# Optimization experiments

Hardware: AMD Instinct MI355X
Metric: run time of the kernel (lower is better)

Reference implementation:

```python
import jax, jax.numpy as jnp
import numpy as np

N = 8192      # num_nodes
B = 16        # batch
IN_DIM = 2    # input_dim
HID = 64      # hid_dim
K = 2         # diffusion_steps
DEG = 16
E = N * DEG
F = IN_DIM + HID            # concat(input, state) feature dim
NUM_MAT = 2 * K + 1         # dual random walk: 2 matrices * K steps + identity


def _spmm(vals, rows, cols, x):
    # sparse [N,N] @ dense [N,M]: y[rows[e]] += vals[e] * x[cols[e]]
    return jax.ops.segment_sum(vals[:, None] * x[cols], rows, num_segments=N)


def _diff_conv(x, W, b, edge_src, edge_dst, vals1, vals2):
    # x: [B, N, F] -> [B, N*out_dim]; Chebyshev-like diffusion recursion
    x0 = jnp.transpose(x, (1, 2, 0)).reshape(N, F * B)  # [N, F*B]
    xs = [x0]
    # matrix 1 = D_out^-1 A (edges src->dst), matrix 2 = D_in^-1 A^T (edges dst->src)
    for rows, cols, vals in ((edge_src, edge_dst, vals1), (edge_dst, edge_src, vals2)):
        x1 = _spmm(vals, rows, cols, x0)
        xs.append(x1)
        xp, xc = x0, x1
        for _ in range(2, K + 1):
            xn = 2.0 * _spmm(vals, rows, cols, xc) - xp
            xs.append(xn)
            xp, xc = xc, xn
    xstk = jnp.stack(xs, 0).reshape(NUM_MAT, N, F, B)
    xstk = jnp.transpose(xstk, (3, 1, 2, 0)).reshape(B * N, F * NUM_MAT)
    out = xstk @ W + b  # [B*N, out_dim]
    return out.reshape(B, -1)


def setup_inputs() -> dict:
    key = jax.random.key(0)
    k = jax.random.split(key, 8)
    inputs = jax.random.normal(k[0], (B, N * IN_DIM), jnp.float32)
    state = jax.random.normal(k[1], (B, N * HID), jnp.float32)
    edge_src = jax.random.randint(k[2], (E,), 0, N)
    edge_dst = jax.random.randint(k[3], (E,), 0, N)
    a = jax.random.uniform(k[4], (E,), jnp.float32) + 0.1  # positive edge weights
    dout = jax.ops.segment_sum(a, edge_src, num_segments=N)
    din = jax.ops.segment_sum(a, edge_dst, num_segments=N)
    vals1 = a / jnp.where(dout > 0, dout, 1.0)[edge_src]  # random-walk normalize A
    vals2 = a / jnp.where(din > 0, din, 1.0)[edge_dst]    # random-walk normalize A^T
    std_g = 1.414 * np.sqrt(2.0 / (F * NUM_MAT + 2 * HID)).astype(np.float32)
    std_c = 1.414 * np.sqrt(2.0 / (F * NUM_MAT + HID)).astype(np.float32)
    W_gate = jax.random.normal(k[5], (F * NUM_MAT, 2 * HID), jnp.float32) * std_g
    b_gate = jnp.zeros((2 * HID,), jnp.float32)
    W_cand = jax.random.normal(k[6], (F * NUM_MAT, HID), jnp.float32) * std_c
    b_cand = jnp.zeros((HID,), jnp.float32)
    return dict(inputs=inputs, state=state, edge_src=edge_src, edge_dst=edge_dst,
                vals1=vals1, vals2=vals2, W_gate=W_gate, b_gate=b_gate,
                W_cand=W_cand, b_cand=b_cand)


def reference(inputs, state, edge_src, edge_dst, vals1, vals2,
              W_gate, b_gate, W_cand, b_cand):
    i = inputs.reshape(B, N, IN_DIM)
    s = state.reshape(B, N, HID)
    x = jnp.concatenate([i, s], axis=2)  # [B, N, F]
    value = jax.nn.sigmoid(_diff_conv(x, W_gate, b_gate, edge_src, edge_dst, vals1, vals2))
    value = value.reshape(B, N, 2 * HID)
    r = value[..., :HID].reshape(B, N * HID)
    u = value[..., HID:].reshape(B, N * HID)
    rs = (r * state).reshape(B, N, HID)
    xc = jnp.concatenate([i, rs], axis=2)
    c = jnp.tanh(_diff_conv(xc, W_cand, b_cand, edge_src, edge_dst, vals1, vals2))
    new_state = u * state + (1.0 - u) * c
    return (new_state, new_state)
```

## Files before the change

kernel.cpp:

```cpp
#include <hip/hip_runtime.h>
#include <cstddef>
#include <cstdint>

#define NNODES 8192
#define BATCH  16
#define HID    64
#define NEDGE  131072
#define SN     524288
#define OUTHALF 8388608
#define FP2    72
#define SLABU  1152
#define NSTR   5760
#define NSTR4  720
#define XCS4   144
#define KP2    384
#define GN     8
#define CWB    288
#define BXB    18432

typedef __attribute__((ext_vector_type(8))) short bf16x8;
typedef __attribute__((ext_vector_type(4))) float f32x4;

static __device__ __forceinline__ float bf2f(ushort u) {
    union { uint32_t i; float f; } c; c.i = ((uint32_t)u) << 16; return c.f;
}
static __device__ __forceinline__ ushort f2bf(float f) {
    union { float f; uint32_t i; } c; c.f = f;
    uint32_t lsb = (c.i >> 16) & 1;
    return (ushort)((c.i + 0x7fffu + lsb) >> 16);
}


__global__ void hist_kernel(const int* __restrict__ src, const int* __restrict__ dst,
                            int* __restrict__ c1, int* __restrict__ c2) {
    int e = blockIdx.x * 256 + threadIdx.x;
    if (e < NEDGE) {
        atomicAdd(&c1[src[e]], 1);
        atomicAdd(&c2[dst[e]], 1);
    }
}

__global__ __launch_bounds__(1024) void scan_kernel(const int* __restrict__ counts1,
                                                    const int* __restrict__ counts2,
                                                    int* __restrict__ rowptr1,
                                                    int* __restrict__ rowptr2,
                                                    int* __restrict__ cursor1,
                                                    int* __restrict__ cursor2) {
    const int* counts = blockIdx.x ? counts2 : counts1;
    int* rowptr       = blockIdx.x ? rowptr2 : rowptr1;
    int* cursor       = blockIdx.x ? cursor2 : cursor1;
    __shared__ int sh[1024];
    int tid = threadIdx.x;
    int base = tid * 8;
    int local[8];
    int sum = 0;
#pragma unroll
    for (int j = 0; j < 8; ++j) { local[j] = counts[base + j]; sum += local[j]; }
    sh[tid] = sum;
    __syncthreads();
    for (int off = 1; off < 1024; off <<= 1) {
        int v = (tid >= off) ? sh[tid - off] : 0;
        __syncthreads();
        sh[tid] += v;
        __syncthreads();
    }
    int p = sh[tid] - sum;
#pragma unroll
    for (int j = 0; j < 8; ++j) {
        cursor[base + j] = p;
        p += local[j];
        rowptr[base + j + 1] = p;
    }
    if (tid == 0) rowptr[0] = 0;
}

__global__ void scatter_kernel(const int* __restrict__ src, const int* __restrict__ dst,
                               const float* __restrict__ v1, const float* __restrict__ v2,
                               int* __restrict__ cur1, int* __restrict__ cur2,
                               int* __restrict__ cols1, float* __restrict__ valsC1,
                               int* __restrict__ cols2, float* __restrict__ valsC2) {
    int e = blockIdx.x * 256 + threadIdx.x;
    if (e < NEDGE) {
        int r1 = src[e];
        int p1 = atomicAdd(&cur1[r1], 1);
        cols1[p1] = dst[e];
        valsC1[p1] = v1[e];
        int r2 = dst[e];
        int p2 = atomicAdd(&cur2[r2], 1);
        cols2[p2] = src[e];
        valsC2[p2] = v2[e];
    }
}


__global__ void prep_kernel(const float* __restrict__ Wg, const float* __restrict__ Wc,
                            ushort* __restrict__ WgT, ushort* __restrict__ WcT,
                            const float* __restrict__ inputs, const float* __restrict__ state,
                            uint* __restrict__ Xb_u, uint* __restrict__ Xc_u) {
    if (blockIdx.x < CWB) {
        int i = blockIdx.x * 256 + threadIdx.x;
        if (i >= 192 * KP2) return;
        int col = i / KP2, k2 = i - col * KP2;
        int m = k2 / FP2, f = k2 - m * FP2;
        bool valid = (m < 5) && (f < 66);
        int ko = f * 5 + m;
        if (col < 128) {
            WgT[col * KP2 + k2] = valid ? f2bf(Wg[ko * 128 + col]) : (ushort)0;
        } else {
            int c = col - 128;
            WcT[c * KP2 + k2] = valid ? f2bf(Wc[ko * 64 + c]) : (ushort)0;
        }
        return;
    }
    int t = (blockIdx.x - CWB) * 256 + threadIdx.x;
    if (t >= NNODES * BATCH * 36) return;
    int n = t / 576;
    int r = t - n * 576;
    int b = r / 36;
    int j = r - b * 36;
    int f0 = 2 * j;
    uint val = 0;
    if (f0 == 0) {
        float v0 = inputs[(size_t)b * (NNODES * 2) + n * 2 + 0];
        float v1 = inputs[(size_t)b * (NNODES * 2) + n * 2 + 1];
        val = (uint)f2bf(v0) | ((uint)f2bf(v1) << 16);
    } else if (f0 < 66) {
        float v0 = state[(size_t)b * SN + n * HID + (f0 - 2)];
        float v1 = state[(size_t)b * SN + n * HID + (f0 - 1)];
        val = (uint)f2bf(v0) | ((uint)f2bf(v1) << 16);
    }
    Xb_u[(size_t)n * 2880 + r] = val;
    if (f0 == 0 || f0 >= 66) Xc_u[t] = val;
}


static __device__ __forceinline__ void fma8(float* acc, uint4 d, float v) {
    acc[0] += v * bf2f((ushort)(d.x));  acc[1] += v * bf2f((ushort)(d.x >> 16));
    acc[2] += v * bf2f((ushort)(d.y));  acc[3] += v * bf2f((ushort)(d.y >> 16));
    acc[4] += v * bf2f((ushort)(d.z));  acc[5] += v * bf2f((ushort)(d.z >> 16));
    acc[6] += v * bf2f((ushort)(d.w));  acc[7] += v * bf2f((ushort)(d.w >> 16));
}

static __device__ __forceinline__ uint4 blend_pack8(const float* acc, uint4 p,
                                                    float alpha, float beta) {
    float o[8];
    o[0] = alpha * acc[0] + beta * bf2f((ushort)(p.x));
    o[1] = alpha * acc[1] + beta * bf2f((ushort)(p.x >> 16));
    o[2] = alpha * acc[2] + beta * bf2f((ushort)(p.y));
    o[3] = alpha * acc[3] + beta * bf2f((ushort)(p.y >> 16));
    o[4] = alpha * acc[4] + beta * bf2f((ushort)(p.z));
    o[5] = alpha * acc[5] + beta * bf2f((ushort)(p.z >> 16));
    o[6] = alpha * acc[6] + beta * bf2f((ushort)(p.w));
    o[7] = alpha * acc[7] + beta * bf2f((ushort)(p.w >> 16));
    uint4 r;
    r.x = (uint32_t)f2bf(o[0]) | ((uint32_t)f2bf(o[1]) << 16);
    r.y = (uint32_t)f2bf(o[2]) | ((uint32_t)f2bf(o[3]) << 16);
    r.z = (uint32_t)f2bf(o[4]) | ((uint32_t)f2bf(o[5]) << 16);
    r.w = (uint32_t)f2bf(o[6]) | ((uint32_t)f2bf(o[7]) << 16);
    return r;
}

__global__ __launch_bounds__(128) void spmm_dual(
        const int* __restrict__ rp1, const int* __restrict__ c1, const float* __restrict__ v1,
        const uint4* __restrict__ x1,
        const int* __restrict__ rp2, const int* __restrict__ c2, const float* __restrict__ v2,
        const uint4* __restrict__ x2,
        int xs,
        const uint4* __restrict__ xp, int ps,
        uint4* __restrict__ y1, uint4* __restrict__ y2, int ys,
        float alpha, float beta) {
    int bid = blockIdx.x;
    int half = bid >> 13;
    int n = bid & 8191;
    const int* rowptr = half ? rp2 : rp1;
    const int* cols   = half ? c2 : c1;
    const float* vals = half ? v2 : v1;
    const uint4* x    = half ? x2 : x1;
    uint4* y          = half ? y2 : y1;

    int t = threadIdx.x;
    int s = rowptr[n], e = rowptr[n + 1];
    float a0[8] = {0, 0, 0, 0, 0, 0, 0, 0};
    float a1[8] = {0, 0, 0, 0, 0, 0, 0, 0};
    bool tail = t < 16;
    int t2 = 128 + t;
    for (int i = s; i < e; i += 8) {
        int   c[8];
        float v[8];
#pragma unroll
        for (int k = 0; k < 8; ++k) {
            int ii = i + k;
            bool ok = ii < e;
            int idx = ok ? ii : s;
            c[k] = cols[idx];
            v[k] = ok ? vals[idx] : 0.f;
        }
        uint4 d[8];
#pragma unroll
        for (int k = 0; k < 8; ++k) d[k] = x[(size_t)c[k] * xs + t];
        uint4 d2[8];
        if (tail) {
#pragma unroll
            for (int k = 0; k < 8; ++k) d2[k] = x[(size_t)c[k] * xs + t2];
        }
#pragma unroll
        for (int k = 0; k < 8; ++k) fma8(a0, d[k], v[k]);
        if (tail) {
#pragma unroll
            for (int k = 0; k < 8; ++k) fma8(a1, d2[k], v[k]);
        }
    }
    uint4* yb = y + (size_t)n * ys;
    const uint4* xpb = xp + (size_t)n * ps;
    uint4 p0 = (beta != 0.f) ? xpb[t] : make_uint4(0, 0, 0, 0);
    yb[t] = blend_pack8(a0, p0, alpha, beta);
    if (tail) {
        uint4 p1 = (beta != 0.f) ? xpb[t2] : make_uint4(0, 0, 0, 0);
        yb[t2] = blend_pack8(a1, p1, alpha, beta);
    }
}


__global__ __launch_bounds__(256, 2) void gate_mfma(const ushort* __restrict__ Xb,
                                                    const ushort* __restrict__ WgT,
                                                    const float* __restrict__ bg,
                                                    float* __restrict__ U,
                                                    ushort* __restrict__ Xc) {
    int tid = threadIdx.x;
    int wave = tid >> 6, lane = tid & 63;
    int row = lane & 15, quad = lane >> 4;
    int c0 = wave * 32 + row;
    int c1 = c0 + 16;

    bf16x8 w0[12], w1[12];
#pragma unroll
    for (int kt = 0; kt < 12; ++kt) {
        w0[kt] = *(const bf16x8*)(WgT + (size_t)c0 * KP2 + kt * 32 + quad * 8);
        w1[kt] = *(const bf16x8*)(WgT + (size_t)c1 * KP2 + kt * 32 + quad * 8);
    }
    float bias0 = bg[c0], bias1 = bg[c1];

    int offA[11];
#pragma unroll
    for (int kt = 0; kt < 11; ++kt) {
        int j = 4 * kt + quad;
        int m = j / 9;
        int f0 = 8 * (j - 9 * m);
        offA[kt] = m * SLABU + row * FP2 + f0;
    }
    int off11 = 4 * SLABU + row * FP2 + 64;
    const bf16x8 zf = {0, 0, 0, 0, 0, 0, 0, 0};

    int nodeBase = blockIdx.x * GN;
    bf16x8 aC[12], aN[12];
    {
        const ushort* An = Xb + (size_t)nodeBase * NSTR;
#pragma unroll
        for (int kt = 0; kt < 11; ++kt) aC[kt] = *(const bf16x8*)(An + offA[kt]);
        aC[11] = (quad == 0) ? *(const bf16x8*)(An + off11) : zf;
    }
    for (int g = 0; g < GN; ++g) {
        int n = nodeBase + g;
        const ushort* An = Xb + (size_t)n * NSTR;
        if (g + 1 < GN) {
            const ushort* An2 = An + NSTR;
#pragma unroll
            for (int kt = 0; kt < 11; ++kt) aN[kt] = *(const bf16x8*)(An2 + offA[kt]);
            aN[11] = (quad == 0) ? *(const bf16x8*)(An2 + off11) : zf;
        }
        f32x4 acc0 = {0.f, 0.f, 0.f, 0.f};
        f32x4 acc1 = {0.f, 0.f, 0.f, 0.f};
#pragma unroll
        for (int kt = 0; kt < 12; ++kt) {
            acc0 = __builtin_amdgcn_mfma_f32_16x16x32_bf16(aC[kt], w0[kt], acc0, 0, 0, 0);
            acc1 = __builtin_amdgcn_mfma_f32_16x16x32_bf16(aC[kt], w1[kt], acc1, 0, 0, 0);
        }
#pragma unroll
        for (int r = 0; r < 4; ++r) {
            int b = quad * 4 + r;
            float v0 = 1.f / (1.f + __expf(-(acc0[r] + bias0)));
            float v1 = 1.f / (1.f + __expf(-(acc1[r] + bias1)));
            if (wave < 2) {
                float s0 = bf2f(An[b * FP2 + 2 + c0]);
                float s1 = bf2f(An[b * FP2 + 2 + c1]);
                Xc[(size_t)n * SLABU + b * FP2 + 2 + c0] = f2bf(v0 * s0);
                Xc[(size_t)n * SLABU + b * FP2 + 2 + c1] = f2bf(v1 * s1);
            } else {
                U[(size_t)b * SN + n * HID + (c0 - HID)] = v0;
                U[(size_t)b * SN + n * HID + (c1 - HID)] = v1;
            }
        }
        if (g + 1 < GN) {
#pragma unroll
            for (int kt = 0; kt < 12; ++kt) aC[kt] = aN[kt];
        }
    }
}


__global__ __launch_bounds__(256, 2) void cand_mfma(const ushort* __restrict__ Xb,
                                                    const ushort* __restrict__ Xc,
                                                    const ushort* __restrict__ WcT,
                                                    const float* __restrict__ bc,
                                                    const float* __restrict__ state,
                                                    const float* U,
                                                    float* out) {
    int tid = threadIdx.x;
    int wave = tid >> 6, lane = tid & 63;
    int row = lane & 15, quad = lane >> 4;
    int c = wave * 16 + row;

    bf16x8 w[12];
#pragma unroll
    for (int kt = 0; kt < 12; ++kt)
        w[kt] = *(const bf16x8*)(WcT + (size_t)c * KP2 + kt * 32 + quad * 8);
    float bias = bc[c];

    int offA[11];
#pragma unroll
    for (int kt = 0; kt < 11; ++kt) {
        int j = 4 * kt + quad;
        int m = j / 9;
        int f0 = 8 * (j - 9 * m);
        offA[kt] = m * SLABU + row * FP2 + f0;
    }
    int off11 = 4 * SLABU + row * FP2 + 64;
    const bf16x8 zf = {0, 0, 0, 0, 0, 0, 0, 0};

    int nodeBase = blockIdx.x * GN;
    bf16x8 aC[12], aN[12];
    auto loadA = [&](int n, bf16x8* a) {
        const ushort* AnB = Xb + (size_t)n * NSTR;
        const ushort* AnC = Xc + (size_t)n * SLABU;
#pragma unroll
        for (int kt = 0; kt < 11; ++kt) {
            const ushort* bp = (kt < 2) ? AnC
                             : (kt == 2 ? (quad == 0 ? AnC : AnB) : AnB);
            a[kt] = *(const bf16x8*)(bp + offA[kt]);
        }
        a[11] = (quad == 0) ? *(const bf16x8*)(AnB + off11) : zf;
    };
    loadA(nodeBase, aC);
    for (int g = 0; g < GN; ++g) {
        int n = nodeBase + g;
        if (g + 1 < GN) loadA(n + 1, aN);
        f32x4 acc = {0.f, 0.f, 0.f, 0.f};
#pragma unroll
        for (int kt = 0; kt < 12; ++kt)
            acc = __builtin_amdgcn_mfma_f32_16x16x32_bf16(aC[kt], w[kt], acc, 0, 0, 0);
#pragma unroll
        for (int r = 0; r < 4; ++r) {
            int b = quad * 4 + r;
            float pre = acc[r] + bias;
            float cv = 1.f - 2.f / (__expf(2.f * pre) + 1.f);
            size_t idx = (size_t)b * SN + n * HID + c;
            float uv = U[idx];
            float s = state[idx];
            float ns = uv * s + (1.f - uv) * cv;
            out[idx] = ns;
            out[OUTHALF + idx] = ns;
        }
        if (g + 1 < GN) {
#pragma unroll
            for (int kt = 0; kt < 12; ++kt) aC[kt] = aN[kt];
        }
    }
}


extern "C" void kernel_launch(void* const* d_in, const int* in_sizes, int n_in,
                              void* d_out, int out_size, void* d_ws, size_t ws_size,
                              hipStream_t stream) {
    const float* inputs = (const float*)d_in[0];
    const float* state  = (const float*)d_in[1];
    const int*   esrc   = (const int*)d_in[2];
    const int*   edst   = (const int*)d_in[3];
    const float* v1     = (const float*)d_in[4];
    const float* v2     = (const float*)d_in[5];
    const float* Wg     = (const float*)d_in[6];
    const float* bg     = (const float*)d_in[7];
    const float* Wc     = (const float*)d_in[8];
    const float* bc     = (const float*)d_in[9];
    float* out = (float*)d_out;

    char* ws = (char*)d_ws;
    size_t off = 0;
    auto alloc = [&](size_t bytes) -> void* {
        void* p = ws + off;
        off += (bytes + 255) & ~(size_t)255;
        return p;
    };
    ushort* Xb     = (ushort*)alloc((size_t)NNODES * NSTR * 2);
    ushort* Xc     = (ushort*)alloc((size_t)NNODES * SLABU * 2);
    ushort* WgT    = (ushort*)alloc((size_t)128 * KP2 * 2);
    ushort* WcT    = (ushort*)alloc((size_t)64 * KP2 * 2);
    int*   counts1 = (int*)alloc(NNODES * 4);
    int*   counts2 = (int*)alloc(NNODES * 4);
    int*   rowptr1 = (int*)alloc((NNODES + 1) * 4);
    int*   rowptr2 = (int*)alloc((NNODES + 1) * 4);
    int*   cursor1 = (int*)alloc(NNODES * 4);
    int*   cursor2 = (int*)alloc(NNODES * 4);
    int*   cols1   = (int*)alloc(NEDGE * 4);
    int*   cols2   = (int*)alloc(NEDGE * 4);
    float* valsC1  = (float*)alloc(NEDGE * 4);
    float* valsC2  = (float*)alloc(NEDGE * 4);

    float* U = out + OUTHALF;

    uint4* Xb4 = (uint4*)Xb;
    uint4* Xc4 = (uint4*)Xc;
    auto slab = [&](int m) { return Xb4 + (size_t)m * 144; };

    hipMemsetAsync(counts1, 0, (size_t)2 * NNODES * 4, stream);
    hist_kernel<<<(NEDGE + 255) / 256, 256, 0, stream>>>(esrc, edst, counts1, counts2);
    scan_kernel<<<2, 1024, 0, stream>>>(counts1, counts2, rowptr1, rowptr2, cursor1, cursor2);
    scatter_kernel<<<(NEDGE + 255) / 256, 256, 0, stream>>>(esrc, edst, v1, v2,
                                                            cursor1, cursor2,
                                                            cols1, valsC1, cols2, valsC2);

    prep_kernel<<<CWB + BXB, 256, 0, stream>>>(Wg, Wc, WgT, WcT,
                                               inputs, state, (uint*)Xb, (uint*)Xc);

    spmm_dual<<<2 * NNODES, 128, 0, stream>>>(rowptr1, cols1, valsC1, slab(0),
                                              rowptr2, cols2, valsC2, slab(0), NSTR4,
                                              slab(0), NSTR4, slab(1), slab(3), NSTR4,
                                              1.f, 0.f);
    spmm_dual<<<2 * NNODES, 128, 0, stream>>>(rowptr1, cols1, valsC1, slab(1),
                                              rowptr2, cols2, valsC2, slab(3), NSTR4,
                                              slab(0), NSTR4, slab(2), slab(4), NSTR4,
                                              2.f, -1.f);

    gate_mfma<<<NNODES / GN, 256, 0, stream>>>(Xb, WgT, bg, U, Xc);

    spmm_dual<<<2 * NNODES, 128, 0, stream>>>(rowptr1, cols1, valsC1, Xc4,
                                              rowptr2, cols2, valsC2, Xc4, XCS4,
                                              Xc4, XCS4, slab(1), slab(3), NSTR4,
                                              1.f, 0.f);
    spmm_dual<<<2 * NNODES, 128, 0, stream>>>(rowptr1, cols1, valsC1, slab(1),
                                              rowptr2, cols2, valsC2, slab(3), NSTR4,
                                              Xc4, XCS4, slab(2), slab(4), NSTR4,
                                              2.f, -1.f);

    cand_mfma<<<NNODES / GN, 256, 0, stream>>>(Xb, Xc, WcT, bc, state, U, out);
}
```

Before: 554.5 us.

## Store SpMM gather operands as packed FP8 copies to halve gather bandwidth

```diff
diff --git a/kernel.cpp b/kernel.cpp
--- a/kernel.cpp
+++ b/kernel.cpp
@@ -1,4 +1,5 @@
 #include <hip/hip_runtime.h>
+#include <hip/hip_fp8.h>
 #include <cstddef>
 #include <cstdint>
 
@@ -17,6 +18,7 @@
 #define GN     8
 #define CWB    288
 #define BXB    18432
+#define FRB    9437184
 
 typedef __attribute__((ext_vector_type(8))) short bf16x8;
 typedef __attribute__((ext_vector_type(4))) float f32x4;
@@ -28,6 +30,12 @@
     union { float f; uint32_t i; } c; c.f = f;
     uint32_t lsb = (c.i >> 16) & 1;
     return (ushort)((c.i + 0x7fffu + lsb) >> 16);
+}
+static __device__ __forceinline__ float fp8tof(uint b) {
+    __hip_fp8_e4m3 h; h.__x = (__hip_fp8_storage_t)(b & 0xffu); return (float)h;
+}
+static __device__ __forceinline__ uint ftofp8(float f) {
+    __hip_fp8_e4m3 h(f); return (uint)h.__x;
 }
 
 
@@ -96,7 +104,8 @@
 __global__ void prep_kernel(const float* __restrict__ Wg, const float* __restrict__ Wc,
                             ushort* __restrict__ WgT, ushort* __restrict__ WcT,
                             const float* __restrict__ inputs, const float* __restrict__ state,
-                            uint* __restrict__ Xb_u, uint* __restrict__ Xc_u) {
+                            uint* __restrict__ Xb_u, uint* __restrict__ Xc_u,
+                            ushort* __restrict__ F0_us) {
     if (blockIdx.x < CWB) {
         int i = blockIdx.x * 256 + threadIdx.x;
         if (i >= 192 * KP2) return;
@@ -119,31 +128,33 @@
     int b = r / 36;
     int j = r - b * 36;
     int f0 = 2 * j;
+    float v0 = 0.f, v1 = 0.f;
     uint val = 0;
     if (f0 == 0) {
-        float v0 = inputs[(size_t)b * (NNODES * 2) + n * 2 + 0];
-        float v1 = inputs[(size_t)b * (NNODES * 2) + n * 2 + 1];
+        v0 = inputs[(size_t)b * (NNODES * 2) + n * 2 + 0];
+        v1 = inputs[(size_t)b * (NNODES * 2) + n * 2 + 1];
         val = (uint)f2bf(v0) | ((uint)f2bf(v1) << 16);
     } else if (f0 < 66) {
-        float v0 = state[(size_t)b * SN + n * HID + (f0 - 2)];
-        float v1 = state[(size_t)b * SN + n * HID + (f0 - 1)];
+        v0 = state[(size_t)b * SN + n * HID + (f0 - 2)];
+        v1 = state[(size_t)b * SN + n * HID + (f0 - 1)];
         val = (uint)f2bf(v0) | ((uint)f2bf(v1) << 16);
     }
     Xb_u[(size_t)n * 2880 + r] = val;
     if (f0 == 0 || f0 >= 66) Xc_u[t] = val;
-}
-
-
-static __device__ __forceinline__ void fma8(float* acc, uint4 d, float v) {
-    acc[0] += v * bf2f((ushort)(d.x));  acc[1] += v * bf2f((ushort)(d.x >> 16));
-    acc[2] += v * bf2f((ushort)(d.y));  acc[3] += v * bf2f((ushort)(d.y >> 16));
-    acc[4] += v * bf2f((ushort)(d.z));  acc[5] += v * bf2f((ushort)(d.z >> 16));
-    acc[6] += v * bf2f((ushort)(d.w));  acc[7] += v * bf2f((ushort)(d.w >> 16));
-}
-
-static __device__ __forceinline__ uint4 blend_pack8(const float* acc, uint4 p,
-                                                    float alpha, float beta) {
-    float o[8];
+    F0_us[t] = (ushort)(ftofp8(v0) | (ftofp8(v1) << 8));
+}
+
+
+static __device__ __forceinline__ void fma8f8(float* acc, uint2 d, float v) {
+    uint a = d.x, b = d.y;
+    acc[0] += v * fp8tof(a);        acc[1] += v * fp8tof(a >> 8);
+    acc[2] += v * fp8tof(a >> 16);  acc[3] += v * fp8tof(a >> 24);
+    acc[4] += v * fp8tof(b);        acc[5] += v * fp8tof(b >> 8);
+    acc[6] += v * fp8tof(b >> 16);  acc[7] += v * fp8tof(b >> 24);
+}
+
+static __device__ __forceinline__ void blend8(const float* acc, uint4 p,
+                                              float alpha, float beta, float* o) {
     o[0] = alpha * acc[0] + beta * bf2f((ushort)(p.x));
     o[1] = alpha * acc[1] + beta * bf2f((ushort)(p.x >> 16));
     o[2] = alpha * acc[2] + beta * bf2f((ushort)(p.y));
@@ -152,6 +163,9 @@
     o[5] = alpha * acc[5] + beta * bf2f((ushort)(p.z >> 16));
     o[6] = alpha * acc[6] + beta * bf2f((ushort)(p.w));
     o[7] = alpha * acc[7] + beta * bf2f((ushort)(p.w >> 16));
+}
+
+static __device__ __forceinline__ uint4 packbf8(const float* o) {
     uint4 r;
     r.x = (uint32_t)f2bf(o[0]) | ((uint32_t)f2bf(o[1]) << 16);
     r.y = (uint32_t)f2bf(o[2]) | ((uint32_t)f2bf(o[3]) << 16);
@@ -160,14 +174,20 @@
     return r;
 }
 
+static __device__ __forceinline__ uint2 packf8(const float* o) {
+    uint2 r;
+    r.x = ftofp8(o[0]) | (ftofp8(o[1]) << 8) | (ftofp8(o[2]) << 16) | (ftofp8(o[3]) << 24);
+    r.y = ftofp8(o[4]) | (ftofp8(o[5]) << 8) | (ftofp8(o[6]) << 16) | (ftofp8(o[7]) << 24);
+    return r;
+}
+
 __global__ __launch_bounds__(128) void spmm_dual(
         const int* __restrict__ rp1, const int* __restrict__ c1, const float* __restrict__ v1,
-        const uint4* __restrict__ x1,
         const int* __restrict__ rp2, const int* __restrict__ c2, const float* __restrict__ v2,
-        const uint4* __restrict__ x2,
-        int xs,
+        const uint2* __restrict__ xf1, const uint2* __restrict__ xf2,
         const uint4* __restrict__ xp, int ps,
         uint4* __restrict__ y1, uint4* __restrict__ y2, int ys,
+        uint2* __restrict__ yf1, uint2* __restrict__ yf2,
         float alpha, float beta) {
     int bid = blockIdx.x;
     int half = bid >> 13;
@@ -175,8 +195,9 @@
     const int* rowptr = half ? rp2 : rp1;
     const int* cols   = half ? c2 : c1;
     const float* vals = half ? v2 : v1;
-    const uint4* x    = half ? x2 : x1;
+    const uint2* xf   = half ? xf2 : xf1;
     uint4* y          = half ? y2 : y1;
+    uint2* yf         = half ? yf2 : yf1;
 
     int t = threadIdx.x;
     int s = rowptr[n], e = rowptr[n + 1];
@@ -195,28 +216,33 @@
             c[k] = cols[idx];
             v[k] = ok ? vals[idx] : 0.f;
         }
-        uint4 d[8];
-#pragma unroll
-        for (int k = 0; k < 8; ++k) d[k] = x[(size_t)c[k] * xs + t];
-        uint4 d2[8];
+        uint2 d[8];
+#pragma unroll
+        for (int k = 0; k < 8; ++k) d[k] = xf[(size_t)c[k] * 144 + t];
+        uint2 d2[8];
         if (tail) {
 #pragma unroll
-            for (int k = 0; k < 8; ++k) d2[k] = x[(size_t)c[k] * xs + t2];
-        }
-#pragma unroll
-        for (int k = 0; k < 8; ++k) fma8(a0, d[k], v[k]);
+            for (int k = 0; k < 8; ++k) d2[k] = xf[(size_t)c[k] * 144 + t2];
+        }
+#pragma unroll
+        for (int k = 0; k < 8; ++k) fma8f8(a0, d[k], v[k]);
         if (tail) {
 #pragma unroll
-            for (int k = 0; k < 8; ++k) fma8(a1, d2[k], v[k]);
+            for (int k = 0; k < 8; ++k) fma8f8(a1, d2[k], v[k]);
         }
     }
     uint4* yb = y + (size_t)n * ys;
     const uint4* xpb = xp + (size_t)n * ps;
+    float o[8];
     uint4 p0 = (beta != 0.f) ? xpb[t] : make_uint4(0, 0, 0, 0);
-    yb[t] = blend_pack8(a0, p0, alpha, beta);
+    blend8(a0, p0, alpha, beta, o);
+    yb[t] = packbf8(o);
+    if (yf) yf[(size_t)n * 144 + t] = packf8(o);
     if (tail) {
         uint4 p1 = (beta != 0.f) ? xpb[t2] : make_uint4(0, 0, 0, 0);
-        yb[t2] = blend_pack8(a1, p1, alpha, beta);
+        blend8(a1, p1, alpha, beta, o);
+        yb[t2] = packbf8(o);
+        if (yf) yf[(size_t)n * 144 + t2] = packf8(o);
     }
 }
 
@@ -225,7 +251,8 @@
                                                     const ushort* __restrict__ WgT,
                                                     const float* __restrict__ bg,
                                                     float* __restrict__ U,
-                                                    ushort* __restrict__ Xc) {
+                                                    ushort* __restrict__ Xc,
+                                                    unsigned char* __restrict__ F0b) {
     int tid = threadIdx.x;
     int wave = tid >> 6, lane = tid & 63;
     int row = lane & 15, quad = lane >> 4;
@@ -283,8 +310,11 @@
             if (wave < 2) {
                 float s0 = bf2f(An[b * FP2 + 2 + c0]);
                 float s1 = bf2f(An[b * FP2 + 2 + c1]);
-                Xc[(size_t)n * SLABU + b * FP2 + 2 + c0] = f2bf(v0 * s0);
-                Xc[(size_t)n * SLABU + b * FP2 + 2 + c1] = f2bf(v1 * s1);
+                float x0v = v0 * s0, x1v = v1 * s1;
+                Xc[(size_t)n * SLABU + b * FP2 + 2 + c0] = f2bf(x0v);
+                Xc[(size_t)n * SLABU + b * FP2 + 2 + c1] = f2bf(x1v);
+                F0b[(size_t)n * 1152 + b * FP2 + 2 + c0] = (unsigned char)ftofp8(x0v);
+                F0b[(size_t)n * 1152 + b * FP2 + 2 + c1] = (unsigned char)ftofp8(x1v);
             } else {
                 U[(size_t)b * SN + n * HID + (c0 - HID)] = v0;
                 U[(size_t)b * SN + n * HID + (c1 - HID)] = v1;
@@ -406,6 +436,10 @@
     float* valsC2  = (float*)alloc(NEDGE * 4);
 
     float* U = out + OUTHALF;
+    unsigned char* Fb = (unsigned char*)d_out;
+    uint2* F0 = (uint2*)Fb;
+    uint2* F1 = (uint2*)(Fb + (size_t)FRB);
+    uint2* F2 = (uint2*)(Fb + (size_t)2 * FRB);
 
     uint4* Xb4 = (uint4*)Xb;
     uint4* Xc4 = (uint4*)Xc;
@@ -419,27 +453,32 @@
                                                             cols1, valsC1, cols2, valsC2);
 
     prep_kernel<<<CWB + BXB, 256, 0, stream>>>(Wg, Wc, WgT, WcT,
-                                               inputs, state, (uint*)Xb, (uint*)Xc);
-
-    spmm_dual<<<2 * NNODES, 128, 0, stream>>>(rowptr1, cols1, valsC1, slab(0),
-                                              rowptr2, cols2, valsC2, slab(0), NSTR4,
-                                              slab(0), NSTR4, slab(1), slab(3), NSTR4,
-                                              1.f, 0.f);
-    spmm_dual<<<2 * NNODES, 128, 0, stream>>>(rowptr1, cols1, valsC1, slab(1),
-                                              rowptr2, cols2, valsC2, slab(3), NSTR4,
-                                              slab(0), NSTR4, slab(2), slab(4), NSTR4,
-                                              2.f, -1.f);
-
-    gate_mfma<<<NNODES / GN, 256, 0, stream>>>(Xb, WgT, bg, U, Xc);
-
-    spmm_dual<<<2 * NNODES, 128, 0, stream>>>(rowptr1, cols1, valsC1, Xc4,
-                                              rowptr2, cols2, valsC2, Xc4, XCS4,
-                                              Xc4, XCS4, slab(1), slab(3), NSTR4,
-                                              1.f, 0.f);
-    spmm_dual<<<2 * NNODES, 128, 0, stream>>>(rowptr1, cols1, valsC1, slab(1),
-                                              rowptr2, cols2, valsC2, slab(3), NSTR4,
-                                              Xc4, XCS4, slab(2), slab(4), NSTR4,
-                                              2.f, -1.f);
+                                               inputs, state, (uint*)Xb, (uint*)Xc,
+                                               (ushort*)F0);
+
+    spmm_dual<<<2 * NNODES, 128, 0, stream>>>(rowptr1, cols1, valsC1,
+                                              rowptr2, cols2, valsC2,
+                                              F0, F0, slab(0), NSTR4,
+                                              slab(1), slab(3), NSTR4,
+                                              F1, F2, 1.f, 0.f);
+    spmm_dual<<<2 * NNODES, 128, 0, stream>>>(rowptr1, cols1, valsC1,
+                                              rowptr2, cols2, valsC2,
+                                              F1, F2, slab(0), NSTR4,
+                                              slab(2), slab(4), NSTR4,
+                                              nullptr, nullptr, 2.f, -1.f);
+
+    gate_mfma<<<NNODES / GN, 256, 0, stream>>>(Xb, WgT, bg, U, Xc, Fb);
+
+    spmm_dual<<<2 * NNODES, 128, 0, stream>>>(rowptr1, cols1, valsC1,
+                                              rowptr2, cols2, valsC2,
+                                              F0, F0, Xc4, XCS4,
+                                              slab(1), slab(3), NSTR4,
+                                              F1, F2, 1.f, 0.f);
+    spmm_dual<<<2 * NNODES, 128, 0, stream>>>(rowptr1, cols1, valsC1,
+                                              rowptr2, cols2, valsC2,
+                                              F1, F2, Xc4, XCS4,
+                                              slab(2), slab(4), NSTR4,
+                                              nullptr, nullptr, 2.f, -1.f);
 
     cand_mfma<<<NNODES / GN, 256, 0, stream>>>(Xb, Xc, WcT, bc, state, U, out);
 }
```

After: 529.9 us. 1.05x faster.
